# Kernel tuning notes

Hardware: AMD Instinct MI355X
Metric: run time of the kernel (lower is better)

Reference implementation:

```python
import jax, jax.numpy as jnp
import numpy as np
import math

S, E = 4096, 2048
H = 4 * E  # FFN hidden
EPS = 1e-5


def _ln_all(y):
    # F.layer_norm(y, y.shape): normalize over ALL elements, no affine
    mu = jnp.mean(y)
    var = jnp.mean(jnp.square(y - mu))
    return (y - mu) / jnp.sqrt(var + EPS)


def setup_inputs() -> dict:
    key = jax.random.key(0)
    ks = jax.random.split(key, 12)
    sc = 0.02
    return {
        "x": jax.random.normal(ks[0], (S, E), dtype=jnp.float32),
        "Wq": jax.random.normal(ks[1], (E, E), dtype=jnp.float32) * sc,
        "bq": jnp.zeros((E,), dtype=jnp.float32),
        "Wk": jax.random.normal(ks[2], (E, E), dtype=jnp.float32) * sc,
        "bk": jnp.zeros((E,), dtype=jnp.float32),
        "Wv": jax.random.normal(ks[3], (E, E), dtype=jnp.float32) * sc,
        "bv": jnp.zeros((E,), dtype=jnp.float32),
        "W1": jax.random.normal(ks[4], (E, H), dtype=jnp.float32) * sc,
        "b1": jnp.zeros((H,), dtype=jnp.float32),
        "W2": jax.random.normal(ks[5], (H, E), dtype=jnp.float32) * sc,
        "b2": jnp.zeros((E,), dtype=jnp.float32),
    }


def reference(x, Wq, bq, Wk, bk, Wv, bv, W1, b1, W2, b2):
    # projections
    Q = x @ Wq + bq  # [S, E]
    K = x @ Wk + bk
    V = x @ Wv + bv
    # NOTE: source scales by sqrt(K.size(-2)) == sqrt(seq_len), not head dim
    scale = 1.0 / math.sqrt(x.shape[-2])
    scores = jax.nn.softmax((Q @ K.T) * scale, axis=-1)  # [S, S]
    attn = scores @ V  # [S, E]
    h = _ln_all(x + attn)
    ffn = jax.nn.relu(h @ W1 + b1) @ W2 + b2
    return _ln_all(h + ffn)
```

## Files before the change

### kernel.cpp

```cpp
#include <hip/hip_runtime.h>
#include <cstdint>
#include <cstddef>


constexpr int S = 4096;
constexpr int E = 2048;
constexpr int H = 8192;

typedef __bf16 bf16;
typedef bf16  bf16x8 __attribute__((ext_vector_type(8)));
typedef bf16  bf16x4 __attribute__((ext_vector_type(4)));
typedef float f32x4  __attribute__((ext_vector_type(4)));

typedef __attribute__((address_space(1))) void as1_void;
typedef __attribute__((address_space(3))) void as3_void;

__device__ __forceinline__ void ldg2lds16(const void* g, void* l) {
  __builtin_amdgcn_global_load_lds((as1_void*)g, (as3_void*)l, 16, 0, 0);
}

template <int EPI, bool SPLITK>
__global__ __launch_bounds__(512, 2)
void gemm256(const bf16* __restrict__ A, int lda,
             const bf16* __restrict__ Bt, int ldb,
             bf16* __restrict__ Cb, float* __restrict__ Cf,
             float* __restrict__ Cf2, int ldc,
             const float* __restrict__ bias,
             int M, int N, int K, float scale)
{
  __shared__ bf16 sA[2][256 * 64];
  __shared__ bf16 sB[2][256 * 64];

  const int tid  = threadIdx.x;
  const int lane = tid & 63;
  const int wave = tid >> 6;

  const int nbx = gridDim.x;
  const int nwg = nbx * gridDim.y;
  const int bid = blockIdx.y * nbx + blockIdx.x;
  int wg = (bid & 7) * (nwg >> 3) + (bid >> 3);

  int kh = 0;
  if (SPLITK) { const int hw = nwg >> 1; if (wg >= hw) { kh = 1; wg -= hw; } }
  const int ntx  = N >> 8;
  const int m0   = (wg / ntx) * 256;
  const int n0   = (wg % ntx) * 256;
  const int Keff = SPLITK ? (K >> 1) : K;
  if (SPLITK) { const size_t ko = (size_t)kh * Keff; A += ko; Bt += ko; }

  const int tr  = tid >> 3;
  const int tc  = tid & 7;
  const int gsw = (tc ^ (tr & 7)) * 8;
  const bf16* gA = A  + (size_t)(m0 + tr) * lda + gsw;
  const bf16* gB = Bt + (size_t)(n0 + tr) * ldb + gsw;
  const size_t a64 = (size_t)64 * lda;
  const size_t b64 = (size_t)64 * ldb;

#define STAGE_A(t, g, b) ldg2lds16(gA + ((size_t)(t) << 6) + (size_t)(g) * a64, \
                                   &sA[b][(g) * 4096 + tid * 8])
#define STAGE_B(t, g, b) ldg2lds16(gB + ((size_t)(t) << 6) + (size_t)(g) * b64, \
                                   &sB[b][(g) * 4096 + tid * 8])

  const int fr = lane & 15;
  const int fq = lane >> 4;
  const int p0 = (fq ^ (fr & 7)) * 8;
  const int p1 = p0 ^ 32;
  const int wm = (wave & 1) * 128;
  const int wn = (wave >> 1) * 64;

  const int NT = Keff >> 6;

  STAGE_A(0, 0, 0); STAGE_A(0, 1, 0); STAGE_A(0, 2, 0); STAGE_A(0, 3, 0);
  STAGE_B(0, 0, 0); STAGE_B(0, 1, 0); STAGE_B(0, 2, 0); STAGE_B(0, 3, 0);
  if (NT > 1) {
    STAGE_A(1, 0, 1); STAGE_A(1, 2, 1);
    STAGE_B(1, 0, 1); STAGE_B(1, 1, 1); STAGE_B(1, 2, 1); STAGE_B(1, 3, 1);
    asm volatile("s_waitcnt vmcnt(6)" ::: "memory");
  } else {
    asm volatile("s_waitcnt vmcnt(0)" ::: "memory");
  }
  __builtin_amdgcn_s_barrier();

  f32x4 acc[8][4] = {};

  for (int t = 0; t < NT; ++t) {
    const int bu = t & 1, nx = bu ^ 1;
    const bf16* rA = &sA[bu][(wm + fr) * 64];
    const bf16* rB = &sB[bu][(wn + fr) * 64];
    bf16x8 a0[4], a1[4], bl0[2], bl1[2], bh0[2], bh1[2];

#pragma unroll
    for (int i = 0; i < 4; ++i) {
      a0[i] = *(const bf16x8*)(rA + i * 1024 + p0);
      a1[i] = *(const bf16x8*)(rA + i * 1024 + p1);
    }
#pragma unroll
    for (int j = 0; j < 2; ++j) {
      bl0[j] = *(const bf16x8*)(rB + j * 1024 + p0);
      bl1[j] = *(const bf16x8*)(rB + j * 1024 + p1);
    }
    if (t + 1 < NT) { STAGE_A(t + 1, 1, nx); STAGE_A(t + 1, 3, nx); }
    __builtin_amdgcn_s_barrier();
    asm volatile("s_waitcnt lgkmcnt(0)" ::: "memory");
    __builtin_amdgcn_s_setprio(1);
#pragma unroll
    for (int i = 0; i < 4; ++i)
#pragma unroll
      for (int j = 0; j < 2; ++j) {
        acc[i][j] = __builtin_amdgcn_mfma_f32_16x16x32_bf16(a0[i], bl0[j], acc[i][j], 0, 0, 0);
        acc[i][j] = __builtin_amdgcn_mfma_f32_16x16x32_bf16(a1[i], bl1[j], acc[i][j], 0, 0, 0);
      }
    __builtin_amdgcn_s_setprio(0);
    __builtin_amdgcn_s_barrier();

#pragma unroll
    for (int j = 0; j < 2; ++j) {
      bh0[j] = *(const bf16x8*)(rB + (2 + j) * 1024 + p0);
      bh1[j] = *(const bf16x8*)(rB + (2 + j) * 1024 + p1);
    }
    if (t + 2 < NT) { STAGE_A(t + 2, 0, bu); STAGE_A(t + 2, 2, bu); }
    __builtin_amdgcn_s_barrier();
    asm volatile("s_waitcnt lgkmcnt(0)" ::: "memory");
    __builtin_amdgcn_s_setprio(1);
#pragma unroll
    for (int i = 0; i < 4; ++i)
#pragma unroll
      for (int j = 0; j < 2; ++j) {
        acc[i][2 + j] = __builtin_amdgcn_mfma_f32_16x16x32_bf16(a0[i], bh0[j], acc[i][2 + j], 0, 0, 0);
        acc[i][2 + j] = __builtin_amdgcn_mfma_f32_16x16x32_bf16(a1[i], bh1[j], acc[i][2 + j], 0, 0, 0);
      }
    __builtin_amdgcn_s_setprio(0);
    __builtin_amdgcn_s_barrier();

#pragma unroll
    for (int i = 0; i < 4; ++i) {
      a0[i] = *(const bf16x8*)(rA + 4096 + i * 1024 + p0);
      a1[i] = *(const bf16x8*)(rA + 4096 + i * 1024 + p1);
    }
    if (t + 2 < NT) { STAGE_B(t + 2, 0, bu); STAGE_B(t + 2, 1, bu); }
    __builtin_amdgcn_s_barrier();
    asm volatile("s_waitcnt lgkmcnt(0)" ::: "memory");
    __builtin_amdgcn_s_setprio(1);
#pragma unroll
    for (int i = 0; i < 4; ++i)
#pragma unroll
      for (int j = 0; j < 2; ++j) {
        acc[4 + i][2 + j] = __builtin_amdgcn_mfma_f32_16x16x32_bf16(a0[i], bh0[j], acc[4 + i][2 + j], 0, 0, 0);
        acc[4 + i][2 + j] = __builtin_amdgcn_mfma_f32_16x16x32_bf16(a1[i], bh1[j], acc[4 + i][2 + j], 0, 0, 0);
      }
    __builtin_amdgcn_s_setprio(0);
    __builtin_amdgcn_s_barrier();

    if (t + 2 < NT) { STAGE_B(t + 2, 2, bu); STAGE_B(t + 2, 3, bu); }
    __builtin_amdgcn_s_barrier();
    __builtin_amdgcn_s_setprio(1);
#pragma unroll
    for (int i = 0; i < 4; ++i)
#pragma unroll
      for (int j = 0; j < 2; ++j) {
        acc[4 + i][j] = __builtin_amdgcn_mfma_f32_16x16x32_bf16(a0[i], bl0[j], acc[4 + i][j], 0, 0, 0);
        acc[4 + i][j] = __builtin_amdgcn_mfma_f32_16x16x32_bf16(a1[i], bl1[j], acc[4 + i][j], 0, 0, 0);
      }
    __builtin_amdgcn_s_setprio(0);
    if (t + 2 < NT) {
      asm volatile("s_waitcnt vmcnt(6)" ::: "memory");
    } else if (t + 1 < NT) {
      asm volatile("s_waitcnt vmcnt(0)" ::: "memory");
    }
    __builtin_amdgcn_s_barrier();
  }
#undef STAGE_A
#undef STAGE_B

  const int er = m0 + wm + fq * 4;
  const int ec = n0 + wn + fr;
  float* const dst6 = (EPI == 6) ? (kh ? Cf2 : Cf) : nullptr;
#pragma unroll
  for (int qm = 0; qm < 2; ++qm) {
#pragma unroll
    for (int i = 0; i < 4; ++i) {
#pragma unroll
      for (int r = 0; r < 4; ++r) {
        const int gr = er + qm * 64 + i * 16 + r;
#pragma unroll
        for (int j = 0; j < 4; ++j) {
          const int gc = ec + j * 16;
          const size_t idx = (size_t)gr * ldc + gc;
          float v = acc[qm * 4 + i][j][r];
          if (EPI == 0) {
            Cb[idx] = (bf16)(v + bias[gc]);
          } else if (EPI == 1) {
            Cb[idx] = (bf16)(v + bias[gr]);
          } else if (EPI == 2) {
            Cb[idx] = (bf16)(v * scale);
          } else if (EPI == 4) {
            v += bias[gc];
            Cb[idx] = (bf16)(v > 0.f ? v : 0.f);
          } else {
            dst6[idx] = v;
          }
        }
      }
    }
  }
}

__global__ __launch_bounds__(256)
void combine_ln(const float* __restrict__ y0, const float* __restrict__ y1,
                const float* __restrict__ bias, const float* __restrict__ addf,
                const bf16* __restrict__ addb,
                float* __restrict__ out, float* __restrict__ red,
                int colMask, int total4)
{
  float ls = 0.f, ls2 = 0.f;
  for (int idx = blockIdx.x * 256 + threadIdx.x; idx < total4;
       idx += gridDim.x * 256) {
    const size_t i = (size_t)idx * 4;
    const float4 u0 = *(const float4*)(y0 + i);
    const float4 u1 = *(const float4*)(y1 + i);
    float vx = u0.x + u1.x, vy = u0.y + u1.y, vz = u0.z + u1.z, vw = u0.w + u1.w;
    if (bias) {
      const float4 b = *(const float4*)(bias + (int)(i & colMask));
      vx += b.x; vy += b.y; vz += b.z; vw += b.w;
    }
    if (addf) {
      const float4 a = *(const float4*)(addf + i);
      vx += a.x; vy += a.y; vz += a.z; vw += a.w;
    }
    if (addb) {
      const bf16x4 a = *(const bf16x4*)(addb + i);
      vx += (float)a[0]; vy += (float)a[1]; vz += (float)a[2]; vw += (float)a[3];
    }
    float4 o; o.x = vx; o.y = vy; o.z = vz; o.w = vw;
    *(float4*)(out + i) = o;
    ls  += vx + vy + vz + vw;
    ls2 += vx * vx + vy * vy + vz * vz + vw * vw;
  }
#pragma unroll
  for (int o = 32; o; o >>= 1) {
    ls  += __shfl_xor(ls,  o, 64);
    ls2 += __shfl_xor(ls2, o, 64);
  }
  __shared__ float sr[8];
  const int lane = threadIdx.x & 63, wave = threadIdx.x >> 6;
  if (lane == 0) { sr[wave * 2] = ls; sr[wave * 2 + 1] = ls2; }
  __syncthreads();
  if (threadIdx.x == 0) {
    atomicAdd(red,     sr[0] + sr[2] + sr[4] + sr[6]);
    atomicAdd(red + 1, sr[1] + sr[3] + sr[5] + sr[7]);
  }
}

__global__ __launch_bounds__(256)
void cvt_f32_bf16(const float* __restrict__ src, bf16* __restrict__ dst)
{
  const size_t i = ((size_t)blockIdx.x * 256 + threadIdx.x) * 4;
  const float4 t = *(const float4*)(src + i);
  bf16x4 b;
  b[0] = (bf16)t.x; b[1] = (bf16)t.y; b[2] = (bf16)t.z; b[3] = (bf16)t.w;
  *(bf16x4*)(dst + i) = b;
}

__global__ __launch_bounds__(256)
void transpose_cvt(const float* __restrict__ src, bf16* __restrict__ dst, int R, int C)
{
  __shared__ float tile[32][33];
  const int c0 = blockIdx.x * 32, r0 = blockIdx.y * 32;
  const int tx = threadIdx.x & 31, ty = threadIdx.x >> 5;
#pragma unroll
  for (int rr = ty; rr < 32; rr += 8)
    tile[rr][tx] = src[(size_t)(r0 + rr) * C + (c0 + tx)];
  __syncthreads();
#pragma unroll
  for (int rr = ty; rr < 32; rr += 8)
    dst[(size_t)(c0 + rr) * R + (r0 + tx)] = (bf16)tile[tx][rr];
}

__global__ __launch_bounds__(256)
void concat_bias(const float* __restrict__ a, const float* __restrict__ b,
                 float* __restrict__ o)
{
  const int i = blockIdx.x * 256 + threadIdx.x;
  o[i] = (i < 2048) ? a[i] : b[i - 2048];
}

__global__ __launch_bounds__(256)
void softmax_rows(bf16* __restrict__ P)
{
  const int row  = blockIdx.x;
  bf16* p = P + (size_t)row * 4096;
  const int tid  = threadIdx.x;
  const int lane = tid & 63, wave = tid >> 6;

  bf16x8 c0 = *(const bf16x8*)(p + tid * 16);
  bf16x8 c1 = *(const bf16x8*)(p + tid * 16 + 8);
  float v[16];
#pragma unroll
  for (int i = 0; i < 8; ++i) { v[i] = (float)c0[i]; v[8 + i] = (float)c1[i]; }

  float m = v[0];
#pragma unroll
  for (int i = 1; i < 16; ++i) m = fmaxf(m, v[i]);
#pragma unroll
  for (int o = 32; o; o >>= 1) m = fmaxf(m, __shfl_xor(m, o, 64));
  __shared__ float sred[8];
  if (lane == 0) sred[wave] = m;
  __syncthreads();
  m = fmaxf(fmaxf(sred[0], sred[1]), fmaxf(sred[2], sred[3]));

  float s = 0.f;
#pragma unroll
  for (int i = 0; i < 16; ++i) { v[i] = __expf(v[i] - m); s += v[i]; }
#pragma unroll
  for (int o = 32; o; o >>= 1) s += __shfl_xor(s, o, 64);
  if (lane == 0) sred[4 + wave] = s;
  __syncthreads();
  s = sred[4] + sred[5] + sred[6] + sred[7];

  const float inv = 1.f / s;
  bf16x8 o0, o1;
#pragma unroll
  for (int i = 0; i < 8; ++i) { o0[i] = (bf16)(v[i] * inv); o1[i] = (bf16)(v[8 + i] * inv); }
  *(bf16x8*)(p + tid * 16)     = o0;
  *(bf16x8*)(p + tid * 16 + 8) = o1;
}

__global__ void ln_finalize(float* red, float n)
{
  const float mu  = red[0] / n;
  const float var = red[1] / n - mu * mu;
  red[2] = mu;
  red[3] = rsqrtf(var + 1e-5f);
}

__global__ __launch_bounds__(256)
void ln_apply(const float* __restrict__ y, const float* __restrict__ red,
              float* __restrict__ of, bf16* __restrict__ ob)
{
  const float mu = red[2], rs = red[3];
  const size_t i = ((size_t)blockIdx.x * 256 + threadIdx.x) * 4;
  float4 t = *(const float4*)(y + i);
  t.x = (t.x - mu) * rs; t.y = (t.y - mu) * rs;
  t.z = (t.z - mu) * rs; t.w = (t.w - mu) * rs;
  if (of) *(float4*)(of + i) = t;
  if (ob) {
    bf16x4 b;
    b[0] = (bf16)t.x; b[1] = (bf16)t.y; b[2] = (bf16)t.z; b[3] = (bf16)t.w;
    *(bf16x4*)(ob + i) = b;
  }
}

extern "C" void kernel_launch(void* const* d_in, const int* in_sizes, int n_in,
                              void* d_out, int out_size, void* d_ws, size_t ws_size,
                              hipStream_t stream)
{
  const float* x  = (const float*)d_in[0];
  const float* Wq = (const float*)d_in[1];
  const float* bq = (const float*)d_in[2];
  const float* Wk = (const float*)d_in[3];
  const float* bk = (const float*)d_in[4];
  const float* Wv = (const float*)d_in[5];
  const float* bv = (const float*)d_in[6];
  const float* W1 = (const float*)d_in[7];
  const float* b1 = (const float*)d_in[8];
  const float* W2 = (const float*)d_in[9];
  const float* b2 = (const float*)d_in[10];
  float* out = (float*)d_out;

  const size_t MB = 1ull << 20;
  char* ws = (char*)d_ws;

  bf16*  xb   = (bf16*)(ws);
  bf16*  hb   = xb;
  bf16*  WqkT = (bf16*)(ws + 16 * MB);
  bf16*  WvT  = (bf16*)(ws + 32 * MB);
  bf16*  W1T  = (bf16*)(ws + 40 * MB);
  bf16*  W2T  = (bf16*)(ws + 72 * MB);
  bf16*  QKb  = (bf16*)(ws + 104 * MB);
  float* y1pv = (float*)(ws + 104 * MB);
  bf16*  Pb   = (bf16*)(ws + 136 * MB);
  bf16*  act  = (bf16*)(ws + 104 * MB);
  bf16*  VbT  = (bf16*)(ws + 168 * MB);
  float* y    = (float*)(ws + 184 * MB);
  float* y1f2 = (float*)(ws + 16 * MB);
  float* red  = (float*)(ws + 216 * MB);
  float* bqk  = (float*)(ws + 216 * MB + 4096);

  hipMemsetAsync(red, 0, 32, stream);

  const dim3 blk(256);
  const dim3 blkg(512);
  const int nElemBlocks = (S * E) / 1024;
  const int total4 = (S * E) / 4;

  cvt_f32_bf16<<<dim3(nElemBlocks), blk, 0, stream>>>(x, xb);
  transpose_cvt<<<dim3(E / 32, E / 32), blk, 0, stream>>>(Wq, WqkT, E, E);
  transpose_cvt<<<dim3(E / 32, E / 32), blk, 0, stream>>>(Wk, WqkT + (size_t)E * E, E, E);
  transpose_cvt<<<dim3(E / 32, E / 32), blk, 0, stream>>>(Wv, WvT, E, E);
  transpose_cvt<<<dim3(H / 32, E / 32), blk, 0, stream>>>(W1, W1T, E, H);
  transpose_cvt<<<dim3(E / 32, H / 32), blk, 0, stream>>>(W2, W2T, H, E);
  concat_bias<<<dim3(16), blk, 0, stream>>>(bq, bk, bqk);

  gemm256<0, false><<<dim3(4096 / 256, S / 256), blkg, 0, stream>>>(
      xb, E, WqkT, E, QKb, nullptr, nullptr, 4096, bqk, S, 4096, E, 0.f);
  gemm256<1, false><<<dim3(S / 256, E / 256), blkg, 0, stream>>>(
      WvT, E, xb, E, VbT, nullptr, nullptr, S, bv, E, S, E, 0.f);

  gemm256<2, false><<<dim3(S / 256, S / 256), blkg, 0, stream>>>(
      QKb, 4096, QKb + 2048, 4096, Pb, nullptr, nullptr, S, nullptr,
      S, S, E, 1.0f / 64.0f);
  softmax_rows<<<dim3(S), blk, 0, stream>>>(Pb);

  gemm256<6, true><<<dim3(E / 256, (S / 256) * 2), blkg, 0, stream>>>(
      Pb, S, VbT, S, nullptr, y, y1pv, E, nullptr, S, E, S, 0.f);
  combine_ln<<<dim3(2048), blk, 0, stream>>>(
      y, y1pv, nullptr, x, nullptr, y, red, E - 1, total4);
  ln_finalize<<<1, 1, 0, stream>>>(red, (float)((size_t)S * E));
  ln_apply<<<dim3(nElemBlocks), blk, 0, stream>>>(y, red, nullptr, hb);

  gemm256<4, false><<<dim3(H / 256, S / 256), blkg, 0, stream>>>(
      hb, E, W1T, E, act, nullptr, nullptr, H, b1, S, H, E, 0.f);

  gemm256<6, true><<<dim3(E / 256, (S / 256) * 2), blkg, 0, stream>>>(
      act, H, W2T, H, nullptr, y, y1f2, E, nullptr, S, E, H, 0.f);
  combine_ln<<<dim3(2048), blk, 0, stream>>>(
      y, y1f2, b2, nullptr, hb, y, red + 4, E - 1, total4);
  ln_finalize<<<1, 1, 0, stream>>>(red + 4, (float)((size_t)S * E));
  ln_apply<<<dim3(nElemBlocks), blk, 0, stream>>>(y, red + 4, out, nullptr);
}
```

Measured before the change: 957.4 us.

## Reschedule GEMM phases with sched barriers and split-K the V projection

Inside each K-step of the GEMM main loop, the global-to-LDS stage issues now go before the LDS fragment reads. Most intra-phase barriers and lgkmcnt waits are dropped, and each phase ends with a sched_barrier plus s_barrier, so the compiler can overlap LDS reads with MFMAs. The V projection now runs as a split-K GEMM writing two fp32 partials, and a new combine kernel sums them with the row bias and converts to bf16. This gives the small 2048x4096 grid more workgroups to fill the CUs, at the cost of extra fp32 traffic and one more launch. Removing the lgkmcnt waits leaves correctness to the compiler's implicit waits before the MFMAs.

```diff
diff --git a/kernel.cpp b/kernel.cpp
--- a/kernel.cpp
+++ b/kernel.cpp
@@ -60,6 +60,8 @@
                                    &sA[b][(g) * 4096 + tid * 8])
 #define STAGE_B(t, g, b) ldg2lds16(gB + ((size_t)(t) << 6) + (size_t)(g) * b64, \
                                    &sB[b][(g) * 4096 + tid * 8])
+#define PHASE_END() do { __builtin_amdgcn_sched_barrier(0); \
+                         __builtin_amdgcn_s_barrier(); } while (0)
 
   const int fr = lane & 15;
   const int fq = lane >> 4;
@@ -89,6 +91,7 @@
     const bf16* rB = &sB[bu][(wn + fr) * 64];
     bf16x8 a0[4], a1[4], bl0[2], bl1[2], bh0[2], bh1[2];
 
+    if (t + 1 < NT) { STAGE_A(t + 1, 1, nx); STAGE_A(t + 1, 3, nx); }
 #pragma unroll
     for (int i = 0; i < 4; ++i) {
       a0[i] = *(const bf16x8*)(rA + i * 1024 + p0);
@@ -99,9 +102,6 @@
       bl0[j] = *(const bf16x8*)(rB + j * 1024 + p0);
       bl1[j] = *(const bf16x8*)(rB + j * 1024 + p1);
     }
-    if (t + 1 < NT) { STAGE_A(t + 1, 1, nx); STAGE_A(t + 1, 3, nx); }
-    __builtin_amdgcn_s_barrier();
-    asm volatile("s_waitcnt lgkmcnt(0)" ::: "memory");
     __builtin_amdgcn_s_setprio(1);
 #pragma unroll
     for (int i = 0; i < 4; ++i)
@@ -111,16 +111,14 @@
         acc[i][j] = __builtin_amdgcn_mfma_f32_16x16x32_bf16(a1[i], bl1[j], acc[i][j], 0, 0, 0);
       }
     __builtin_amdgcn_s_setprio(0);
-    __builtin_amdgcn_s_barrier();
-
+    PHASE_END();
+
+    if (t + 2 < NT) { STAGE_A(t + 2, 0, bu); STAGE_A(t + 2, 2, bu); }
 #pragma unroll
     for (int j = 0; j < 2; ++j) {
       bh0[j] = *(const bf16x8*)(rB + (2 + j) * 1024 + p0);
       bh1[j] = *(const bf16x8*)(rB + (2 + j) * 1024 + p1);
     }
-    if (t + 2 < NT) { STAGE_A(t + 2, 0, bu); STAGE_A(t + 2, 2, bu); }
-    __builtin_amdgcn_s_barrier();
-    asm volatile("s_waitcnt lgkmcnt(0)" ::: "memory");
     __builtin_amdgcn_s_setprio(1);
 #pragma unroll
     for (int i = 0; i < 4; ++i)
@@ -130,16 +128,14 @@
         acc[i][2 + j] = __builtin_amdgcn_mfma_f32_16x16x32_bf16(a1[i], bh1[j], acc[i][2 + j], 0, 0, 0);
       }
     __builtin_amdgcn_s_setprio(0);
-    __builtin_amdgcn_s_barrier();
-
+    PHASE_END();
+
+    if (t + 2 < NT) { STAGE_B(t + 2, 0, bu); STAGE_B(t + 2, 1, bu); }
 #pragma unroll
     for (int i = 0; i < 4; ++i) {
       a0[i] = *(const bf16x8*)(rA + 4096 + i * 1024 + p0);
       a1[i] = *(const bf16x8*)(rA + 4096 + i * 1024 + p1);
     }
-    if (t + 2 < NT) { STAGE_B(t + 2, 0, bu); STAGE_B(t + 2, 1, bu); }
-    __builtin_amdgcn_s_barrier();
-    asm volatile("s_waitcnt lgkmcnt(0)" ::: "memory");
     __builtin_amdgcn_s_setprio(1);
 #pragma unroll
     for (int i = 0; i < 4; ++i)
@@ -149,10 +145,9 @@
         acc[4 + i][2 + j] = __builtin_amdgcn_mfma_f32_16x16x32_bf16(a1[i], bh1[j], acc[4 + i][2 + j], 0, 0, 0);
       }
     __builtin_amdgcn_s_setprio(0);
-    __builtin_amdgcn_s_barrier();
+    PHASE_END();
 
     if (t + 2 < NT) { STAGE_B(t + 2, 2, bu); STAGE_B(t + 2, 3, bu); }
-    __builtin_amdgcn_s_barrier();
     __builtin_amdgcn_s_setprio(1);
 #pragma unroll
     for (int i = 0; i < 4; ++i)
@@ -167,10 +162,11 @@
     } else if (t + 1 < NT) {
       asm volatile("s_waitcnt vmcnt(0)" ::: "memory");
     }
-    __builtin_amdgcn_s_barrier();
+    PHASE_END();
   }
 #undef STAGE_A
 #undef STAGE_B
+#undef PHASE_END
 
   const int er = m0 + wm + fq * 4;
   const int ec = n0 + wn + fr;
@@ -189,8 +185,6 @@
           float v = acc[qm * 4 + i][j][r];
           if (EPI == 0) {
             Cb[idx] = (bf16)(v + bias[gc]);
-          } else if (EPI == 1) {
-            Cb[idx] = (bf16)(v + bias[gr]);
           } else if (EPI == 2) {
             Cb[idx] = (bf16)(v * scale);
           } else if (EPI == 4) {
@@ -248,6 +242,26 @@
   if (threadIdx.x == 0) {
     atomicAdd(red,     sr[0] + sr[2] + sr[4] + sr[6]);
     atomicAdd(red + 1, sr[1] + sr[3] + sr[5] + sr[7]);
+  }
+}
+
+__global__ __launch_bounds__(256)
+void combine_bias_row(const float* __restrict__ p0, const float* __restrict__ p1,
+                      const float* __restrict__ bias, bf16* __restrict__ outb,
+                      int shift, int total4)
+{
+  for (int idx = blockIdx.x * 256 + threadIdx.x; idx < total4;
+       idx += gridDim.x * 256) {
+    const size_t i = (size_t)idx * 4;
+    const float4 u0 = *(const float4*)(p0 + i);
+    const float4 u1 = *(const float4*)(p1 + i);
+    const float b = bias[idx >> shift];
+    bf16x4 o;
+    o[0] = (bf16)(u0.x + u1.x + b);
+    o[1] = (bf16)(u0.y + u1.y + b);
+    o[2] = (bf16)(u0.z + u1.z + b);
+    o[3] = (bf16)(u0.w + u1.w + b);
+    *(bf16x4*)(outb + i) = o;
   }
 }
 
@@ -379,9 +393,11 @@
   bf16*  QKb  = (bf16*)(ws + 104 * MB);
   float* y1pv = (float*)(ws + 104 * MB);
   bf16*  Pb   = (bf16*)(ws + 136 * MB);
+  float* vph1 = (float*)(ws + 136 * MB);
   bf16*  act  = (bf16*)(ws + 104 * MB);
   bf16*  VbT  = (bf16*)(ws + 168 * MB);
   float* y    = (float*)(ws + 184 * MB);
+  float* vph0 = (float*)(ws + 184 * MB);
   float* y1f2 = (float*)(ws + 16 * MB);
   float* red  = (float*)(ws + 216 * MB);
   float* bqk  = (float*)(ws + 216 * MB + 4096);
@@ -403,8 +419,11 @@
 
   gemm256<0, false><<<dim3(4096 / 256, S / 256), blkg, 0, stream>>>(
       xb, E, WqkT, E, QKb, nullptr, nullptr, 4096, bqk, S, 4096, E, 0.f);
-  gemm256<1, false><<<dim3(S / 256, E / 256), blkg, 0, stream>>>(
-      WvT, E, xb, E, VbT, nullptr, nullptr, S, bv, E, S, E, 0.f);
+
+  gemm256<6, true><<<dim3(S / 256, (E / 256) * 2), blkg, 0, stream>>>(
+      WvT, E, xb, E, nullptr, vph0, vph1, S, nullptr, E, S, E, 0.f);
+  combine_bias_row<<<dim3(2048), blk, 0, stream>>>(
+      vph0, vph1, bv, VbT, 10, (E * S) / 4);
 
   gemm256<2, false><<<dim3(S / 256, S / 256), blkg, 0, stream>>>(
       QKb, 4096, QKb + 2048, 4096, Pb, nullptr, nullptr, S, nullptr,
```

New measurement: 1.080 ms. 12.8% more time.
